# Performance work log

Hardware: AMD Instinct MI355X
Metric: run time of the kernel (lower is better)

The kernel has to match this reference:

```python
import jax, jax.numpy as jnp
import numpy as np

HIDDEN = 4096
N_HEADS = 32
N_KV_HEADS = 8
HEAD_DIM = HIDDEN // N_HEADS  # 128
GROUPS = N_HEADS // N_KV_HEADS  # 4
ROPE_BASE = 10000.0
BATCH, SEQ = 1, 2048


def _rope_cos_sin(position_ids, dim, base):
    # position_ids: [b, s] int -> cos/sin [b, s, dim]
    inv_freq = 1.0 / (base ** (jnp.arange(0, dim, 2, dtype=jnp.float32) / dim))  # [dim/2]
    freqs = position_ids.astype(jnp.float32)[..., None] * inv_freq  # [b, s, dim/2]
    emb = jnp.concatenate([freqs, freqs], axis=-1)  # [b, s, dim]
    return jnp.cos(emb), jnp.sin(emb)


def _rotate_half(x):
    x1, x2 = jnp.split(x, 2, axis=-1)
    return jnp.concatenate([-x2, x1], axis=-1)


def setup_inputs() -> dict:
    key = jax.random.key(0)
    ks = jax.random.split(key, 8)
    s = 0.02
    return {
        'hidden_states': jax.random.normal(ks[0], (BATCH, SEQ, HIDDEN), dtype=jnp.float32),
        'position_ids': jnp.broadcast_to(jnp.arange(SEQ, dtype=jnp.int64), (BATCH, SEQ)),
        'Wq': jax.random.normal(ks[1], (HIDDEN, N_HEADS * HEAD_DIM), dtype=jnp.float32) * s,
        'bq': jax.random.normal(ks[2], (N_HEADS * HEAD_DIM,), dtype=jnp.float32) * s,
        'Wk': jax.random.normal(ks[3], (HIDDEN, N_KV_HEADS * HEAD_DIM), dtype=jnp.float32) * s,
        'bk': jax.random.normal(ks[4], (N_KV_HEADS * HEAD_DIM,), dtype=jnp.float32) * s,
        'Wv': jax.random.normal(ks[5], (HIDDEN, N_KV_HEADS * HEAD_DIM), dtype=jnp.float32) * s,
        'bv': jax.random.normal(ks[6], (N_KV_HEADS * HEAD_DIM,), dtype=jnp.float32) * s,
        'Wo': jax.random.normal(ks[7], (HIDDEN, HIDDEN), dtype=jnp.float32) * s,
    }


def reference(hidden_states, position_ids, Wq, bq, Wk, bk, Wv, bv, Wo):
    b, s, _ = hidden_states.shape
    # QKV projections (bias=True for q/k/v per module)
    q = hidden_states @ Wq + bq  # [b, s, H*d]
    k = hidden_states @ Wk + bk  # [b, s, Hk*d]
    v = hidden_states @ Wv + bv  # [b, s, Hk*d]
    q = q.reshape(b, s, N_HEADS, HEAD_DIM)
    k = k.reshape(b, s, N_KV_HEADS, HEAD_DIM)
    v = v.reshape(b, s, N_KV_HEADS, HEAD_DIM)

    # RoPE gathered by position_ids
    cos, sin = _rope_cos_sin(position_ids, HEAD_DIM, ROPE_BASE)  # [b, s, d]
    cos = cos[:, :, None, :]
    sin = sin[:, :, None, :]
    q = q * cos + _rotate_half(q) * sin
    k = k * cos + _rotate_half(k) * sin

    # GQA causal attention: group query heads over shared kv heads
    qg = q.reshape(b, s, N_KV_HEADS, GROUPS, HEAD_DIM)
    scale = 1.0 / jnp.sqrt(jnp.asarray(HEAD_DIM, dtype=q.dtype))
    scores = jnp.einsum('bqhgd,bkhd->bhgqk', qg, k) * scale  # [b, Hk, g, s, s]
    causal = jnp.tril(jnp.ones((s, s), dtype=bool))
    scores = jnp.where(causal, scores, jnp.finfo(scores.dtype).min)
    probs = jax.nn.softmax(scores, axis=-1)
    out = jnp.einsum('bhgqk,bkhd->bqhgd', probs, v)  # [b, s, Hk, g, d]
    out = out.reshape(b, s, HIDDEN)
    return out @ Wo  # o_proj, bias=False
```

## Files before the change

### kernel.cpp

```cpp
#include <hip/hip_runtime.h>
#include <hip/hip_bf16.h>

typedef __hip_bfloat16 bf16;
typedef __attribute__((ext_vector_type(8))) __bf16 bf16x8;
typedef __attribute__((ext_vector_type(4))) float f32x4;

#define SEQ 2048
#define HID 4096
#define NH 32
#define NKV 8
#define HD 128
#define KVDIM 1024
#define QKVN 6144

#define MiB (1024 * 1024)
#define SCALE_LOG2E 0.12751743f

__device__ __forceinline__ void gl_lds16(const void* g, void* lds) {
  __builtin_amdgcn_global_load_lds((const __attribute__((address_space(1))) void*)g,
                                   (__attribute__((address_space(3))) void*)lds,
                                   16, 0, 0);
}

__device__ __forceinline__ float unplo(unsigned u) { return __uint_as_float(u << 16); }
__device__ __forceinline__ float unphi(unsigned u) { return __uint_as_float(u & 0xffff0000u); }
__device__ __forceinline__ unsigned packbf(float a, float b) {
  bf16 t[2] = {__float2bfloat16(a), __float2bfloat16(b)};
  return *reinterpret_cast<unsigned*>(t);
}

__global__ void concat_bias_kernel(const float* __restrict__ bq, const float* __restrict__ bk,
                                   const float* __restrict__ bv, float* __restrict__ o) {
  int i = blockIdx.x * blockDim.x + threadIdx.x;
  if (i >= QKVN) return;
  o[i] = (i < HID) ? bq[i] : (i < HID + KVDIM ? bk[i - HID] : bv[i - HID - KVDIM]);
}

__global__ void transpose_all_kernel(const float* __restrict__ Wq, const float* __restrict__ Wk,
                                     const float* __restrict__ Wv, const float* __restrict__ Wo,
                                     bf16* __restrict__ Wqkvt, bf16* __restrict__ Wot,
                                     const float* __restrict__ hidden, bf16* __restrict__ Xb) {
  __shared__ float tile[32][33];
  int t = blockIdx.x;
  if (t >= 40960) {
    int i = ((t - 40960) * 256 + threadIdx.y * 32 + threadIdx.x) * 4;
    float4 v = *reinterpret_cast<const float4*>(hidden + i);
    bf16 o[4] = {__float2bfloat16(v.x), __float2bfloat16(v.y),
                 __float2bfloat16(v.z), __float2bfloat16(v.w)};
    *reinterpret_cast<short4*>(Xb + i) = *reinterpret_cast<const short4*>(o);
    return;
  }
  const float* in;
  bf16* out;
  int si, xt, yt;
  if (t < 16384)      { in = Wq; out = Wqkvt;                           si = HID;   xt = t & 127; yt = t >> 7; }
  else if (t < 20480) { t -= 16384; in = Wk; out = Wqkvt + (size_t)HID * HID;           si = KVDIM; xt = t & 31; yt = t >> 5; }
  else if (t < 24576) { t -= 20480; in = Wv; out = Wqkvt + (size_t)(HID + KVDIM) * HID; si = KVDIM; xt = t & 31; yt = t >> 5; }
  else                { t -= 24576; in = Wo; out = Wot;                 si = HID;   xt = t & 127; yt = t >> 7; }
  int c0 = xt * 32, r0 = yt * 32;
  int tx = threadIdx.x, ty = threadIdx.y;
#pragma unroll
  for (int i = 0; i < 32; i += 8)
    tile[ty + i][tx] = in[(size_t)(r0 + ty + i) * si + (c0 + tx)];
  __syncthreads();
#pragma unroll
  for (int i = 0; i < 32; i += 8)
    out[(size_t)(c0 + ty + i) * HID + (r0 + tx)] = __float2bfloat16(tile[tx][ty + i]);
}

__global__ void postqkv_kernel(const bf16* __restrict__ Ch, bf16* __restrict__ Qb,
                               bf16* __restrict__ Kb, bf16* __restrict__ Vt) {
  __shared__ float tile[32][33];
  int b = blockIdx.x;
  int tid = threadIdx.x;
  if (b < 10240) {
    bool isQ = (b < 8192);
    int idx = (isQ ? b : b - 8192) * 256 + tid;
    int j = idx & 31;
    int h = (idx >> 5) & (isQ ? 31 : 7);
    int s = idx >> (isQ ? 10 : 8);
    size_t bi = (size_t)s * QKVN + (isQ ? 0 : HID) + h * HD;
    unsigned u1 = *reinterpret_cast<const unsigned*>(Ch + bi + 2 * j);
    unsigned u2 = *reinterpret_cast<const unsigned*>(Ch + bi + 64 + 2 * j);
    float x1a = unplo(u1), x1b = unphi(u1);
    float x2a = unplo(u2), x2b = unphi(u2);
    float inv0 = __expf(-(float)(2 * j) * 0.14391156831212787f);
    float inv1 = __expf(-(float)(2 * j + 1) * 0.14391156831212787f);
    float sn0, cs0, sn1, cs1;
    __sincosf((float)s * inv0, &sn0, &cs0);
    __sincosf((float)s * inv1, &sn1, &cs1);
    if (isQ) {
      cs0 *= SCALE_LOG2E; sn0 *= SCALE_LOG2E;
      cs1 *= SCALE_LOG2E; sn1 *= SCALE_LOG2E;
    }
    size_t bo = (size_t)s * (isQ ? HID : KVDIM) + h * HD;
    bf16* Ob = isQ ? Qb : Kb;
    *reinterpret_cast<unsigned*>(Ob + bo + 2 * j) =
        packbf(x1a * cs0 - x2a * sn0, x1b * cs1 - x2b * sn1);
    *reinterpret_cast<unsigned*>(Ob + bo + 64 + 2 * j) =
        packbf(x2a * cs0 + x1a * sn0, x2b * cs1 + x1b * sn1);
  } else {
    int t = b - 10240;
    int xt = t & 31, yt = t >> 5;
    int tx = tid & 31, ty = tid >> 5;
#pragma unroll
    for (int i = 0; i < 32; i += 8)
      tile[ty + i][tx] = __bfloat162float(Ch[(size_t)(yt * 32 + ty + i) * QKVN + (HID + KVDIM) + xt * 32 + tx]);
    __syncthreads();
#pragma unroll
    for (int i = 0; i < 32; i += 8)
      Vt[(size_t)(xt * 32 + ty + i) * SEQ + (yt * 32 + tx)] = __float2bfloat16(tile[tx][ty + i]);
  }
}

#define BARRIER() __builtin_amdgcn_s_barrier()
#define LGKM0()                                          \
  {                                                      \
    asm volatile("s_waitcnt lgkmcnt(0)" ::: "memory");   \
    __builtin_amdgcn_sched_barrier(0);                   \
  }
#define MFMA_ACC(d, x, y) d = __builtin_amdgcn_mfma_f32_16x16x32_bf16(x, y, d, 0, 0, 0)

__global__ __launch_bounds__(512, 2) void qkvgemm_kernel(
    const bf16* __restrict__ A,
    const bf16* __restrict__ Bt,
    const float* __restrict__ bias,
    bf16* __restrict__ Ch) {
  __shared__ bf16 lds[2][448 * 64];
  const int blk = blockIdx.x;
  const int sw = (blk & 7) * 32 + (blk >> 3);
  const int bx = sw & 31, by = sw >> 5;
  const int n0 = bx * 192;
  const int m0 = by * 256;
  const int tid = threadIdx.x;
  const int lane = tid & 63;
  const int w = tid >> 6;
  const int wr = w >> 2, wc = w & 3;
  const int hig = lane >> 4;
  const int nt = HID / 64;

#define QSTAGE_A(buf, t)                                                          \
  {                                                                               \
    _Pragma("unroll")                                                             \
    for (int _c = 0; _c < 4; ++_c) {                                              \
      int _row = _c * 64 + w * 8 + (lane >> 3);                                   \
      int _ch = (lane & 7) ^ ((lane >> 3) & 7);                                   \
      gl_lds16(A + (size_t)(m0 + _row) * HID + (size_t)(t) * 64 + _ch * 8,        \
               &lds[buf][(_c * 64 + w * 8) * 64]);                                \
    }                                                                             \
  }
#define QSTAGE_B(buf, t)                                                          \
  {                                                                               \
    _Pragma("unroll")                                                             \
    for (int _c = 0; _c < 3; ++_c) {                                              \
      int _row = _c * 64 + w * 8 + (lane >> 3);                                   \
      int _ch = (lane & 7) ^ ((lane >> 3) & 7);                                   \
      gl_lds16(Bt + (size_t)(n0 + _row) * HID + (size_t)(t) * 64 + _ch * 8,       \
               &lds[buf][(256 + _c * 64 + w * 8) * 64]);                          \
    }                                                                             \
  }

  auto rdA = [&](int cur, int mi, int ks) {
    int rr = wr * 128 + mi * 16 + (lane & 15);
    int byt = rr * 128 + (((ks * 32 + hig * 8) * 2) ^ ((rr & 7) << 4));
    return *reinterpret_cast<const bf16x8*>(
        reinterpret_cast<const char*>(&lds[cur][0]) + byt);
  };
  auto rdB = [&](int cur, int ni, int ks) {
    int rr = wc * 48 + ni * 16 + (lane & 15);
    int byt = 32768 + rr * 128 + (((ks * 32 + hig * 8) * 2) ^ ((rr & 7) << 4));
    return *reinterpret_cast<const bf16x8*>(
        reinterpret_cast<const char*>(&lds[cur][0]) + byt);
  };

  f32x4 acc[8][3];
  const f32x4 z = {0.f, 0.f, 0.f, 0.f};
#pragma unroll
  for (int i = 0; i < 8; ++i)
#pragma unroll
    for (int j = 0; j < 3; ++j) acc[i][j] = z;

  QSTAGE_A(0, 0); QSTAGE_B(0, 0);
  QSTAGE_B(1, 1);
  asm volatile("s_waitcnt vmcnt(3)" ::: "memory");
  BARRIER();

  bf16x8 a[4][2], b[3][2];
  int cur = 0;
  for (int t = 0; t < nt; ++t, cur ^= 1) {
#pragma unroll
    for (int mi = 0; mi < 4; ++mi) { a[mi][0] = rdA(cur, mi, 0); a[mi][1] = rdA(cur, mi, 1); }
#pragma unroll
    for (int ni = 0; ni < 3; ++ni) { b[ni][0] = rdB(cur, ni, 0); b[ni][1] = rdB(cur, ni, 1); }
    if (t + 1 < nt) QSTAGE_A(cur ^ 1, t + 1);
    LGKM0();
    __builtin_amdgcn_s_setprio(1);
#pragma unroll
    for (int mi = 0; mi < 4; ++mi)
#pragma unroll
      for (int ni = 0; ni < 3; ++ni) {
        MFMA_ACC(acc[mi][ni], a[mi][0], b[ni][0]);
        MFMA_ACC(acc[mi][ni], a[mi][1], b[ni][1]);
      }
    __builtin_amdgcn_s_setprio(0);
    BARRIER();
#pragma unroll
    for (int mi = 0; mi < 4; ++mi) { a[mi][0] = rdA(cur, mi + 4, 0); a[mi][1] = rdA(cur, mi + 4, 1); }
    if (t + 2 < nt) QSTAGE_B(cur, t + 2);
    LGKM0();
    __builtin_amdgcn_s_setprio(1);
#pragma unroll
    for (int mi = 0; mi < 4; ++mi)
#pragma unroll
      for (int ni = 0; ni < 3; ++ni) {
        MFMA_ACC(acc[mi + 4][ni], a[mi][0], b[ni][0]);
        MFMA_ACC(acc[mi + 4][ni], a[mi][1], b[ni][1]);
      }
    __builtin_amdgcn_s_setprio(0);
    if (t + 1 < nt) {
      if (t + 2 < nt) {
        asm volatile("s_waitcnt vmcnt(3)" ::: "memory");
      } else {
        asm volatile("s_waitcnt vmcnt(0)" ::: "memory");
      }
    }
    BARRIER();
  }

#pragma unroll
  for (int ni = 0; ni < 3; ++ni) {
    int col = n0 + wc * 48 + ni * 16 + (lane & 15);
    float bv = bias[col];
#pragma unroll
    for (int mi = 0; mi < 8; ++mi) {
      int rbase = m0 + wr * 128 + mi * 16 + hig * 4;
#pragma unroll
      for (int r = 0; r < 4; ++r)
        Ch[(size_t)(rbase + r) * QKVN + col] = __float2bfloat16(acc[mi][ni][r] + bv);
    }
  }
#undef QSTAGE_A
#undef QSTAGE_B
}

__global__ __launch_bounds__(512, 2) void wogemm_kernel(
    const bf16* __restrict__ A,
    const bf16* __restrict__ Bt,
    float* __restrict__ C) {
  __shared__ bf16 lds[2][3][128 * 64];
  const int blk = blockIdx.x;
  const int sw = (blk & 7) * 32 + (blk >> 3);
  const int n0 = (sw & 31) * 128;
  const int m0 = (sw >> 5) * 256;
  const int tid = threadIdx.x;
  const int lane = tid & 63;
  const int w = tid >> 6;
  const int wr = w >> 1, wc = w & 1;
  const int nt = HID / 64;

#define WSTAGE(buf, slot, t)                                                    \
  {                                                                             \
    const bf16* _s = ((slot) == 2) ? Bt : A;                                    \
    int _g0 = ((slot) == 2) ? n0 : (m0 + (slot) * 128);                         \
    _Pragma("unroll")                                                           \
    for (int _it = 0; _it < 2; ++_it) {                                         \
      int _row = w * 16 + _it * 8 + (lane >> 3);                                \
      int _ch = (lane & 7) ^ (_row & 7);                                        \
      gl_lds16(_s + (size_t)(_g0 + _row) * HID + (size_t)(t) * 64 + _ch * 8,    \
               &lds[buf][slot][(w * 16 + _it * 8) * 64]);                       \
    }                                                                           \
  }

  auto rdA = [&](int cur, int mi, int ks) {
    int rr = (wr & 1) * 64 + mi * 16 + (lane & 15);
    int byt = rr * 128 + (((ks * 32 + (lane >> 4) * 8) * 2) ^ ((rr & 7) << 4));
    return *reinterpret_cast<const bf16x8*>(
        reinterpret_cast<const char*>(&lds[cur][wr >> 1][0]) + byt);
  };
  auto rdB = [&](int cur, int ni, int ks) {
    int rr = wc * 64 + ni * 16 + (lane & 15);
    int byt = rr * 128 + (((ks * 32 + (lane >> 4) * 8) * 2) ^ ((rr & 7) << 4));
    return *reinterpret_cast<const bf16x8*>(
        reinterpret_cast<const char*>(&lds[cur][2][0]) + byt);
  };

  f32x4 acc[4][4];
  const f32x4 z = {0.f, 0.f, 0.f, 0.f};
#pragma unroll
  for (int i = 0; i < 4; ++i)
#pragma unroll
    for (int j = 0; j < 4; ++j) acc[i][j] = z;

  WSTAGE(0, 0, 0); WSTAGE(0, 1, 0); WSTAGE(0, 2, 0);
  WSTAGE(1, 2, 1);
  asm volatile("s_waitcnt vmcnt(2)" ::: "memory");
  BARRIER();

  bf16x8 a[2][2], b[4][2];
  int cur = 0;
  for (int t = 0; t < nt; ++t, cur ^= 1) {
#pragma unroll
    for (int mi = 0; mi < 2; ++mi) { a[mi][0] = rdA(cur, mi, 0); a[mi][1] = rdA(cur, mi, 1); }
#pragma unroll
    for (int ni = 0; ni < 4; ++ni) { b[ni][0] = rdB(cur, ni, 0); b[ni][1] = rdB(cur, ni, 1); }
    if (t + 1 < nt) { WSTAGE(cur ^ 1, 0, t + 1); WSTAGE(cur ^ 1, 1, t + 1); }
    LGKM0();
    __builtin_amdgcn_s_setprio(1);
#pragma unroll
    for (int mi = 0; mi < 2; ++mi)
#pragma unroll
      for (int ni = 0; ni < 4; ++ni) {
        MFMA_ACC(acc[mi][ni], a[mi][0], b[ni][0]);
        MFMA_ACC(acc[mi][ni], a[mi][1], b[ni][1]);
      }
    __builtin_amdgcn_s_setprio(0);
    BARRIER();
#pragma unroll
    for (int mi = 0; mi < 2; ++mi) { a[mi][0] = rdA(cur, mi + 2, 0); a[mi][1] = rdA(cur, mi + 2, 1); }
    if (t + 2 < nt) WSTAGE(cur, 2, t + 2);
    LGKM0();
    __builtin_amdgcn_s_setprio(1);
#pragma unroll
    for (int mi = 0; mi < 2; ++mi)
#pragma unroll
      for (int ni = 0; ni < 4; ++ni) {
        MFMA_ACC(acc[mi + 2][ni], a[mi][0], b[ni][0]);
        MFMA_ACC(acc[mi + 2][ni], a[mi][1], b[ni][1]);
      }
    __builtin_amdgcn_s_setprio(0);
    if (t + 1 < nt) {
      if (t + 2 < nt) {
        asm volatile("s_waitcnt vmcnt(2)" ::: "memory");
      } else {
        asm volatile("s_waitcnt vmcnt(0)" ::: "memory");
      }
    }
    BARRIER();
  }

#pragma unroll
  for (int ni = 0; ni < 4; ++ni) {
    int col = n0 + wc * 64 + ni * 16 + (lane & 15);
#pragma unroll
    for (int mi = 0; mi < 4; ++mi) {
      int rbase = m0 + wr * 64 + mi * 16 + (lane >> 4) * 4;
#pragma unroll
      for (int r = 0; r < 4; ++r)
        C[(size_t)(rbase + r) * HID + col] = acc[mi][ni][r];
    }
  }
#undef WSTAGE
}

__global__ __launch_bounds__(256) void attn_kernel(
    const bf16* __restrict__ Q, const bf16* __restrict__ Kb,
    const bf16* __restrict__ Vt, bf16* __restrict__ AO,
    float* __restrict__ Opart, float* __restrict__ Ml) {
  __shared__ bf16 Ks[64 * 128];
  __shared__ bf16 Vs[128 * 64];
  __shared__ bf16 Ps[4][16 * 64];
  const int tid = threadIdx.x, lane = tid & 63, w = tid >> 6;
  const int b = blockIdx.x;
  const int H = b & 31;
  const int tt = b >> 5;
  int qb, lo, hi, half;
  bool split;
  if (tt < 32) {
    qb = 16 + ((31 - tt) >> 1);
    half = tt & 1;
    int n = qb + 1, mid = n >> 1;
    lo = half ? mid : 0;
    hi = half ? n : mid;
    split = true;
  } else {
    qb = 47 - tt;
    half = 0;
    lo = 0;
    hi = qb + 1;
    split = false;
  }
  const int kvh = H >> 2;
  const int qw = qb * 64 + w * 16;
  const int hig = lane >> 4;
  const int q_loc = lane & 15;
  const int qa = qw + q_loc;

  bf16x8 aq[4];
#pragma unroll
  for (int kd = 0; kd < 4; ++kd) {
    int row = qw + q_loc;
    int d = kd * 32 + hig * 8;
    aq[kd] = *reinterpret_cast<const bf16x8*>(Q + (size_t)row * HID + H * HD + d);
  }

  float m_run = -1e30f, l_run = 0.0f;
  f32x4 o[8];
  const f32x4 z = {0.f, 0.f, 0.f, 0.f};
#pragma unroll
  for (int dt = 0; dt < 8; ++dt) o[dt] = z;

  for (int t = lo; t < hi; ++t) {
    int kvbase = t * 64;
#pragma unroll
    for (int it = 0; it < 4; ++it) {
      int c = w * 4 + it;
      int row = c * 4 + (lane >> 4);
      int sb = ((lane & 15) * 16) ^ ((row & 7) << 4);
      gl_lds16(Kb + (size_t)(kvbase + row) * KVDIM + kvh * HD + (sb >> 1), &Ks[c * 512]);
    }
#pragma unroll
    for (int it = 0; it < 4; ++it) {
      int c = w * 4 + it;
      int row = c * 8 + (lane >> 3);
      int sb = ((lane & 7) * 16) ^ ((row & 7) << 4);
      gl_lds16(Vt + (size_t)(kvh * HD + row) * SEQ + kvbase + (sb >> 1), &Vs[c * 512]);
    }
    __syncthreads();

    f32x4 sf[4];
#pragma unroll
    for (int j = 0; j < 4; ++j) sf[j] = z;
#pragma unroll
    for (int j = 0; j < 4; ++j) {
#pragma unroll
      for (int kd = 0; kd < 4; ++kd) {
        int r = j * 16 + q_loc;
        int byt = r * 256 + (((kd * 32 + hig * 8) * 2) ^ ((r & 7) << 4));
        bf16x8 kfr = *reinterpret_cast<const bf16x8*>(reinterpret_cast<const char*>(Ks) + byt);
        sf[j] = __builtin_amdgcn_mfma_f32_16x16x32_bf16(kfr, aq[kd], sf[j], 0, 0, 0);
      }
    }

    float vals[4][4];
    bool diag = (t == qb);
#pragma unroll
    for (int j = 0; j < 4; ++j)
#pragma unroll
      for (int r = 0; r < 4; ++r) {
        float v = sf[j][r];
        if (diag) {
          int ka = kvbase + j * 16 + hig * 4 + r;
          if (ka > qa) v = -1e30f;
        }
        vals[j][r] = v;
      }

    float m01 = fmaxf(fmaxf(vals[0][0], vals[0][1]), fmaxf(vals[0][2], vals[0][3]));
    float m23 = fmaxf(fmaxf(vals[1][0], vals[1][1]), fmaxf(vals[1][2], vals[1][3]));
    float m45 = fmaxf(fmaxf(vals[2][0], vals[2][1]), fmaxf(vals[2][2], vals[2][3]));
    float m67 = fmaxf(fmaxf(vals[3][0], vals[3][1]), fmaxf(vals[3][2], vals[3][3]));
    float m = fmaxf(fmaxf(m01, m23), fmaxf(m45, m67));
    m = fmaxf(m, __shfl_xor(m, 16));
    m = fmaxf(m, __shfl_xor(m, 32));
    float m_old = m_run;
    float mn = fmaxf(m_old, m);
    m_run = mn;
    float alpha = __builtin_exp2f(m_old - mn);

    float p[4][4];
    float rs = 0.0f;
#pragma unroll
    for (int j = 0; j < 4; ++j)
#pragma unroll
      for (int r = 0; r < 4; ++r) {
        p[j][r] = __builtin_exp2f(vals[j][r] - mn);
        rs += p[j][r];
      }
    rs += __shfl_xor(rs, 16);
    rs += __shfl_xor(rs, 32);
    l_run = l_run * alpha + rs;

#pragma unroll
    for (int j = 0; j < 4; ++j) {
      bf16 tmp[4] = {__float2bfloat16(p[j][0]), __float2bfloat16(p[j][1]),
                     __float2bfloat16(p[j][2]), __float2bfloat16(p[j][3])};
      int coff = (j * 16 + hig * 4) * 2;
      int byt = q_loc * 128 + (coff ^ ((q_loc & 7) << 4));
      *reinterpret_cast<uint2*>(reinterpret_cast<char*>(&Ps[w][0]) + byt) =
          *reinterpret_cast<const uint2*>(tmp);
    }

    if (__any(mn > m_old)) {
#pragma unroll
      for (int r = 0; r < 4; ++r) {
        float alr = __shfl(alpha, hig * 4 + r);
#pragma unroll
        for (int dt = 0; dt < 8; ++dt) o[dt][r] *= alr;
      }
    }

    bf16x8 pa[2];
#pragma unroll
    for (int ks = 0; ks < 2; ++ks) {
      int byt = q_loc * 128 + (((ks * 32 + hig * 8) * 2) ^ ((q_loc & 7) << 4));
      pa[ks] = *reinterpret_cast<const bf16x8*>(reinterpret_cast<const char*>(&Ps[w][0]) + byt);
    }
#pragma unroll
    for (int dt = 0; dt < 8; ++dt)
#pragma unroll
      for (int ks = 0; ks < 2; ++ks) {
        int vrow = dt * 16 + q_loc;
        int byt = vrow * 128 + (((ks * 32 + hig * 8) * 2) ^ ((vrow & 7) << 4));
        bf16x8 vb = *reinterpret_cast<const bf16x8*>(reinterpret_cast<const char*>(Vs) + byt);
        o[dt] = __builtin_amdgcn_mfma_f32_16x16x32_bf16(pa[ks], vb, o[dt], 0, 0, 0);
      }
    __syncthreads();
  }

  if (!split) {
#pragma unroll
    for (int r = 0; r < 4; ++r) {
      float li = __shfl(l_run, hig * 4 + r);
      float linv = 1.0f / li;
#pragma unroll
      for (int dt = 0; dt < 8; ++dt) {
        int qrow = qw + hig * 4 + r;
        int d = dt * 16 + q_loc;
        AO[(size_t)qrow * HID + H * HD + d] = __float2bfloat16(o[dt][r] * linv);
      }
    }
  } else {
    size_t pbase = ((size_t)(half * NH + H) * 1024);
#pragma unroll
    for (int dt = 0; dt < 8; ++dt)
#pragma unroll
      for (int r = 0; r < 4; ++r) {
        int qrow = qw + hig * 4 + r;
        int d = dt * 16 + q_loc;
        Opart[(pbase + (qrow - 1024)) * HD + d] = o[dt][r];
      }
    if (lane < 16) {
      Ml[(pbase + (qa - 1024)) * 2 + 0] = m_run;
      Ml[(pbase + (qa - 1024)) * 2 + 1] = l_run;
    }
  }
}

__global__ __launch_bounds__(256) void merge_kernel(
    const float* __restrict__ Opart, const float* __restrict__ Ml,
    bf16* __restrict__ AO) {
  int i = blockIdx.x * 256 + threadIdx.x;
  int dq = (i & 31) << 2;
  int row = (i >> 5) & 1023;
  int H = i >> 15;
  size_t b1 = (size_t)H * 1024 + row;
  size_t b2 = (size_t)(NH + H) * 1024 + row;
  float m1 = Ml[b1 * 2], l1 = Ml[b1 * 2 + 1];
  float m2 = Ml[b2 * 2], l2 = Ml[b2 * 2 + 1];
  float M = fmaxf(m1, m2);
  float w1 = __builtin_exp2f(m1 - M), w2 = __builtin_exp2f(m2 - M);
  float inv = 1.0f / (l1 * w1 + l2 * w2);
  float4 o1 = *reinterpret_cast<const float4*>(Opart + b1 * HD + dq);
  float4 o2 = *reinterpret_cast<const float4*>(Opart + b2 * HD + dq);
  bf16 o[4] = {__float2bfloat16((o1.x * w1 + o2.x * w2) * inv),
               __float2bfloat16((o1.y * w1 + o2.y * w2) * inv),
               __float2bfloat16((o1.z * w1 + o2.z * w2) * inv),
               __float2bfloat16((o1.w * w1 + o2.w * w2) * inv)};
  *reinterpret_cast<short4*>(AO + (size_t)(1024 + row) * HID + H * HD + dq) =
      *reinterpret_cast<const short4*>(o);
}

extern "C" void kernel_launch(void* const* d_in, const int* in_sizes, int n_in,
                              void* d_out, int out_size, void* d_ws, size_t ws_size,
                              hipStream_t stream) {
  const float* hidden = (const float*)d_in[0];
  const float* Wq = (const float*)d_in[2];
  const float* bq = (const float*)d_in[3];
  const float* Wk = (const float*)d_in[4];
  const float* bk = (const float*)d_in[5];
  const float* Wv = (const float*)d_in[6];
  const float* bv = (const float*)d_in[7];
  const float* Wo = (const float*)d_in[8];
  float* out = (float*)d_out;

  char* ws = (char*)d_ws;
  bf16*  Wqkvt  = (bf16*)(ws + (size_t)0 * MiB);
  bf16*  Xb     = (bf16*)(ws + (size_t)48 * MiB);
  bf16*  Cqkvh  = (bf16*)(ws + (size_t)64 * MiB);
  bf16*  Wot    = (bf16*)(ws + (size_t)88 * MiB);
  bf16*  Qb     = (bf16*)(ws + (size_t)120 * MiB);
  bf16*  Kb     = (bf16*)(ws + (size_t)136 * MiB);
  bf16*  Vt     = (bf16*)(ws + (size_t)140 * MiB);
  float* bqkv   = (float*)Qb;
  bf16*  AO     = Cqkvh;
  float* Opart  = (float*)Wqkvt;
  float* Ml     = (float*)(ws + (size_t)48 * MiB);

  concat_bias_kernel<<<QKVN / 256, 256, 0, stream>>>(bq, bk, bv, bqkv);
  transpose_all_kernel<<<49152, dim3(32, 8), 0, stream>>>(
      Wq, Wk, Wv, Wo, Wqkvt, Wot, hidden, Xb);

  qkvgemm_kernel<<<256, 512, 0, stream>>>(Xb, Wqkvt, bqkv, Cqkvh);

  postqkv_kernel<<<12288, 256, 0, stream>>>(Cqkvh, Qb, Kb, Vt);

  attn_kernel<<<1536, 256, 0, stream>>>(Qb, Kb, Vt, AO, Opart, Ml);
  merge_kernel<<<(NH * 1024 * 32) / 256, 256, 0, stream>>>(Opart, Ml, AO);

  wogemm_kernel<<<256, 512, 0, stream>>>(AO, Wot, out);
}
```

Before: 317.3 us.

## Replace split-KV attention with paired query-block scheduling and drop merge kernel

The attention work split changes. Before, long query blocks were split into two KV halves with partial outputs merged by a separate kernel. Now each block processes a pair of query blocks (pr and 31-pr) in two sequential passes, which gives every block the same causal work. This removes the fp32 partial writes, the merge kernel launch and its memory traffic. In exchange the grid shrinks from 1536 to 512 blocks, each running longer serial loops, which may reduce occupancy and latency hiding on 256 CUs.

```diff
diff --git a/kernel.cpp b/kernel.cpp
--- a/kernel.cpp
+++ b/kernel.cpp
@@ -354,160 +354,146 @@
 
 __global__ __launch_bounds__(256) void attn_kernel(
     const bf16* __restrict__ Q, const bf16* __restrict__ Kb,
-    const bf16* __restrict__ Vt, bf16* __restrict__ AO,
-    float* __restrict__ Opart, float* __restrict__ Ml) {
+    const bf16* __restrict__ Vt, bf16* __restrict__ AO) {
   __shared__ bf16 Ks[64 * 128];
   __shared__ bf16 Vs[128 * 64];
   __shared__ bf16 Ps[4][16 * 64];
   const int tid = threadIdx.x, lane = tid & 63, w = tid >> 6;
   const int b = blockIdx.x;
   const int H = b & 31;
-  const int tt = b >> 5;
-  int qb, lo, hi, half;
-  bool split;
-  if (tt < 32) {
-    qb = 16 + ((31 - tt) >> 1);
-    half = tt & 1;
-    int n = qb + 1, mid = n >> 1;
-    lo = half ? mid : 0;
-    hi = half ? n : mid;
-    split = true;
-  } else {
-    qb = 47 - tt;
-    half = 0;
-    lo = 0;
-    hi = qb + 1;
-    split = false;
-  }
+  const int pr = b >> 5;
   const int kvh = H >> 2;
-  const int qw = qb * 64 + w * 16;
   const int hig = lane >> 4;
   const int q_loc = lane & 15;
-  const int qa = qw + q_loc;
-
-  bf16x8 aq[4];
-#pragma unroll
-  for (int kd = 0; kd < 4; ++kd) {
-    int row = qw + q_loc;
-    int d = kd * 32 + hig * 8;
-    aq[kd] = *reinterpret_cast<const bf16x8*>(Q + (size_t)row * HID + H * HD + d);
-  }
-
-  float m_run = -1e30f, l_run = 0.0f;
-  f32x4 o[8];
   const f32x4 z = {0.f, 0.f, 0.f, 0.f};
-#pragma unroll
-  for (int dt = 0; dt < 8; ++dt) o[dt] = z;
-
-  for (int t = lo; t < hi; ++t) {
-    int kvbase = t * 64;
-#pragma unroll
-    for (int it = 0; it < 4; ++it) {
-      int c = w * 4 + it;
-      int row = c * 4 + (lane >> 4);
-      int sb = ((lane & 15) * 16) ^ ((row & 7) << 4);
-      gl_lds16(Kb + (size_t)(kvbase + row) * KVDIM + kvh * HD + (sb >> 1), &Ks[c * 512]);
-    }
-#pragma unroll
-    for (int it = 0; it < 4; ++it) {
-      int c = w * 4 + it;
-      int row = c * 8 + (lane >> 3);
-      int sb = ((lane & 7) * 16) ^ ((row & 7) << 4);
-      gl_lds16(Vt + (size_t)(kvh * HD + row) * SEQ + kvbase + (sb >> 1), &Vs[c * 512]);
-    }
-    __syncthreads();
-
-    f32x4 sf[4];
-#pragma unroll
-    for (int j = 0; j < 4; ++j) sf[j] = z;
-#pragma unroll
-    for (int j = 0; j < 4; ++j) {
-#pragma unroll
-      for (int kd = 0; kd < 4; ++kd) {
-        int r = j * 16 + q_loc;
-        int byt = r * 256 + (((kd * 32 + hig * 8) * 2) ^ ((r & 7) << 4));
-        bf16x8 kfr = *reinterpret_cast<const bf16x8*>(reinterpret_cast<const char*>(Ks) + byt);
-        sf[j] = __builtin_amdgcn_mfma_f32_16x16x32_bf16(kfr, aq[kd], sf[j], 0, 0, 0);
-      }
-    }
-
-    float vals[4][4];
-    bool diag = (t == qb);
-#pragma unroll
-    for (int j = 0; j < 4; ++j)
-#pragma unroll
-      for (int r = 0; r < 4; ++r) {
-        float v = sf[j][r];
-        if (diag) {
-          int ka = kvbase + j * 16 + hig * 4 + r;
-          if (ka > qa) v = -1e30f;
+
+#pragma unroll
+  for (int pass = 0; pass < 2; ++pass) {
+    const int qb = pass ? (31 - pr) : pr;
+    const int qw = qb * 64 + w * 16;
+    const int qa = qw + q_loc;
+
+    bf16x8 aq[4];
+#pragma unroll
+    for (int kd = 0; kd < 4; ++kd) {
+      int row = qw + q_loc;
+      int d = kd * 32 + hig * 8;
+      aq[kd] = *reinterpret_cast<const bf16x8*>(Q + (size_t)row * HID + H * HD + d);
+    }
+
+    float m_run = -1e30f, l_run = 0.0f;
+    f32x4 o[8];
+#pragma unroll
+    for (int dt = 0; dt < 8; ++dt) o[dt] = z;
+
+    for (int t = 0; t <= qb; ++t) {
+      int kvbase = t * 64;
+#pragma unroll
+      for (int it = 0; it < 4; ++it) {
+        int c = w * 4 + it;
+        int row = c * 4 + (lane >> 4);
+        int sb = ((lane & 15) * 16) ^ ((row & 7) << 4);
+        gl_lds16(Kb + (size_t)(kvbase + row) * KVDIM + kvh * HD + (sb >> 1), &Ks[c * 512]);
+      }
+#pragma unroll
+      for (int it = 0; it < 4; ++it) {
+        int c = w * 4 + it;
+        int row = c * 8 + (lane >> 3);
+        int sb = ((lane & 7) * 16) ^ ((row & 7) << 4);
+        gl_lds16(Vt + (size_t)(kvh * HD + row) * SEQ + kvbase + (sb >> 1), &Vs[c * 512]);
+      }
+      __syncthreads();
+
+      f32x4 sf[4];
+#pragma unroll
+      for (int j = 0; j < 4; ++j) sf[j] = z;
+#pragma unroll
+      for (int j = 0; j < 4; ++j) {
+#pragma unroll
+        for (int kd = 0; kd < 4; ++kd) {
+          int r = j * 16 + q_loc;
+          int byt = r * 256 + (((kd * 32 + hig * 8) * 2) ^ ((r & 7) << 4));
+          bf16x8 kfr = *reinterpret_cast<const bf16x8*>(reinterpret_cast<const char*>(Ks) + byt);
+          sf[j] = __builtin_amdgcn_mfma_f32_16x16x32_bf16(kfr, aq[kd], sf[j], 0, 0, 0);
         }
-        vals[j][r] = v;
-      }
-
-    float m01 = fmaxf(fmaxf(vals[0][0], vals[0][1]), fmaxf(vals[0][2], vals[0][3]));
-    float m23 = fmaxf(fmaxf(vals[1][0], vals[1][1]), fmaxf(vals[1][2], vals[1][3]));
-    float m45 = fmaxf(fmaxf(vals[2][0], vals[2][1]), fmaxf(vals[2][2], vals[2][3]));
-    float m67 = fmaxf(fmaxf(vals[3][0], vals[3][1]), fmaxf(vals[3][2], vals[3][3]));
-    float m = fmaxf(fmaxf(m01, m23), fmaxf(m45, m67));
-    m = fmaxf(m, __shfl_xor(m, 16));
-    m = fmaxf(m, __shfl_xor(m, 32));
-    float m_old = m_run;
-    float mn = fmaxf(m_old, m);
-    m_run = mn;
-    float alpha = __builtin_exp2f(m_old - mn);
-
-    float p[4][4];
-    float rs = 0.0f;
-#pragma unroll
-    for (int j = 0; j < 4; ++j)
-#pragma unroll
-      for (int r = 0; r < 4; ++r) {
-        p[j][r] = __builtin_exp2f(vals[j][r] - mn);
-        rs += p[j][r];
-      }
-    rs += __shfl_xor(rs, 16);
-    rs += __shfl_xor(rs, 32);
-    l_run = l_run * alpha + rs;
-
-#pragma unroll
-    for (int j = 0; j < 4; ++j) {
-      bf16 tmp[4] = {__float2bfloat16(p[j][0]), __float2bfloat16(p[j][1]),
-                     __float2bfloat16(p[j][2]), __float2bfloat16(p[j][3])};
-      int coff = (j * 16 + hig * 4) * 2;
-      int byt = q_loc * 128 + (coff ^ ((q_loc & 7) << 4));
-      *reinterpret_cast<uint2*>(reinterpret_cast<char*>(&Ps[w][0]) + byt) =
-          *reinterpret_cast<const uint2*>(tmp);
-    }
-
-    if (__any(mn > m_old)) {
-#pragma unroll
-      for (int r = 0; r < 4; ++r) {
-        float alr = __shfl(alpha, hig * 4 + r);
-#pragma unroll
-        for (int dt = 0; dt < 8; ++dt) o[dt][r] *= alr;
-      }
-    }
-
-    bf16x8 pa[2];
-#pragma unroll
-    for (int ks = 0; ks < 2; ++ks) {
-      int byt = q_loc * 128 + (((ks * 32 + hig * 8) * 2) ^ ((q_loc & 7) << 4));
-      pa[ks] = *reinterpret_cast<const bf16x8*>(reinterpret_cast<const char*>(&Ps[w][0]) + byt);
-    }
-#pragma unroll
-    for (int dt = 0; dt < 8; ++dt)
+      }
+
+      float vals[4][4];
+      bool diag = (t == qb);
+#pragma unroll
+      for (int j = 0; j < 4; ++j)
+#pragma unroll
+        for (int r = 0; r < 4; ++r) {
+          float v = sf[j][r];
+          if (diag) {
+            int ka = kvbase + j * 16 + hig * 4 + r;
+            if (ka > qa) v = -1e30f;
+          }
+          vals[j][r] = v;
+        }
+
+      float m01 = fmaxf(fmaxf(vals[0][0], vals[0][1]), fmaxf(vals[0][2], vals[0][3]));
+      float m23 = fmaxf(fmaxf(vals[1][0], vals[1][1]), fmaxf(vals[1][2], vals[1][3]));
+      float m45 = fmaxf(fmaxf(vals[2][0], vals[2][1]), fmaxf(vals[2][2], vals[2][3]));
+      float m67 = fmaxf(fmaxf(vals[3][0], vals[3][1]), fmaxf(vals[3][2], vals[3][3]));
+      float m = fmaxf(fmaxf(m01, m23), fmaxf(m45, m67));
+      m = fmaxf(m, __shfl_xor(m, 16));
+      m = fmaxf(m, __shfl_xor(m, 32));
+      float m_old = m_run;
+      float mn = fmaxf(m_old, m);
+      m_run = mn;
+      float alpha = __builtin_exp2f(m_old - mn);
+
+      float p[4][4];
+      float rs = 0.0f;
+#pragma unroll
+      for (int j = 0; j < 4; ++j)
+#pragma unroll
+        for (int r = 0; r < 4; ++r) {
+          p[j][r] = __builtin_exp2f(vals[j][r] - mn);
+          rs += p[j][r];
+        }
+      rs += __shfl_xor(rs, 16);
+      rs += __shfl_xor(rs, 32);
+      l_run = l_run * alpha + rs;
+
+#pragma unroll
+      for (int j = 0; j < 4; ++j) {
+        bf16 tmp[4] = {__float2bfloat16(p[j][0]), __float2bfloat16(p[j][1]),
+                       __float2bfloat16(p[j][2]), __float2bfloat16(p[j][3])};
+        int coff = (j * 16 + hig * 4) * 2;
+        int byt = q_loc * 128 + (coff ^ ((q_loc & 7) << 4));
+        *reinterpret_cast<uint2*>(reinterpret_cast<char*>(&Ps[w][0]) + byt) =
+            *reinterpret_cast<const uint2*>(tmp);
+      }
+
+      if (__any(mn > m_old)) {
+#pragma unroll
+        for (int r = 0; r < 4; ++r) {
+          float alr = __shfl(alpha, hig * 4 + r);
+#pragma unroll
+          for (int dt = 0; dt < 8; ++dt) o[dt][r] *= alr;
+        }
+      }
+
+      bf16x8 pa[2];
 #pragma unroll
       for (int ks = 0; ks < 2; ++ks) {
-        int vrow = dt * 16 + q_loc;
-        int byt = vrow * 128 + (((ks * 32 + hig * 8) * 2) ^ ((vrow & 7) << 4));
-        bf16x8 vb = *reinterpret_cast<const bf16x8*>(reinterpret_cast<const char*>(Vs) + byt);
-        o[dt] = __builtin_amdgcn_mfma_f32_16x16x32_bf16(pa[ks], vb, o[dt], 0, 0, 0);
-      }
-    __syncthreads();
-  }
-
-  if (!split) {
+        int byt = q_loc * 128 + (((ks * 32 + hig * 8) * 2) ^ ((q_loc & 7) << 4));
+        pa[ks] = *reinterpret_cast<const bf16x8*>(reinterpret_cast<const char*>(&Ps[w][0]) + byt);
+      }
+#pragma unroll
+      for (int dt = 0; dt < 8; ++dt)
+#pragma unroll
+        for (int ks = 0; ks < 2; ++ks) {
+          int vrow = dt * 16 + q_loc;
+          int byt = vrow * 128 + (((ks * 32 + hig * 8) * 2) ^ ((vrow & 7) << 4));
+          bf16x8 vb = *reinterpret_cast<const bf16x8*>(reinterpret_cast<const char*>(Vs) + byt);
+          o[dt] = __builtin_amdgcn_mfma_f32_16x16x32_bf16(pa[ks], vb, o[dt], 0, 0, 0);
+        }
+      __syncthreads();
+    }
+
 #pragma unroll
     for (int r = 0; r < 4; ++r) {
       float li = __shfl(l_run, hig * 4 + r);
@@ -519,45 +505,7 @@
         AO[(size_t)qrow * HID + H * HD + d] = __float2bfloat16(o[dt][r] * linv);
       }
     }
-  } else {
-    size_t pbase = ((size_t)(half * NH + H) * 1024);
-#pragma unroll
-    for (int dt = 0; dt < 8; ++dt)
-#pragma unroll
-      for (int r = 0; r < 4; ++r) {
-        int qrow = qw + hig * 4 + r;
-        int d = dt * 16 + q_loc;
-        Opart[(pbase + (qrow - 1024)) * HD + d] = o[dt][r];
-      }
-    if (lane < 16) {
-      Ml[(pbase + (qa - 1024)) * 2 + 0] = m_run;
-      Ml[(pbase + (qa - 1024)) * 2 + 1] = l_run;
-    }
-  }
-}
-
-__global__ __launch_bounds__(256) void merge_kernel(
-    const float* __restrict__ Opart, const float* __restrict__ Ml,
-    bf16* __restrict__ AO) {
-  int i = blockIdx.x * 256 + threadIdx.x;
-  int dq = (i & 31) << 2;
-  int row = (i >> 5) & 1023;
-  int H = i >> 15;
-  size_t b1 = (size_t)H * 1024 + row;
-  size_t b2 = (size_t)(NH + H) * 1024 + row;
-  float m1 = Ml[b1 * 2], l1 = Ml[b1 * 2 + 1];
-  float m2 = Ml[b2 * 2], l2 = Ml[b2 * 2 + 1];
-  float M = fmaxf(m1, m2);
-  float w1 = __builtin_exp2f(m1 - M), w2 = __builtin_exp2f(m2 - M);
-  float inv = 1.0f / (l1 * w1 + l2 * w2);
-  float4 o1 = *reinterpret_cast<const float4*>(Opart + b1 * HD + dq);
-  float4 o2 = *reinterpret_cast<const float4*>(Opart + b2 * HD + dq);
-  bf16 o[4] = {__float2bfloat16((o1.x * w1 + o2.x * w2) * inv),
-               __float2bfloat16((o1.y * w1 + o2.y * w2) * inv),
-               __float2bfloat16((o1.z * w1 + o2.z * w2) * inv),
-               __float2bfloat16((o1.w * w1 + o2.w * w2) * inv)};
-  *reinterpret_cast<short4*>(AO + (size_t)(1024 + row) * HID + H * HD + dq) =
-      *reinterpret_cast<const short4*>(o);
+  }
 }
 
 extern "C" void kernel_launch(void* const* d_in, const int* in_sizes, int n_in,
@@ -583,8 +531,6 @@
   bf16*  Vt     = (bf16*)(ws + (size_t)140 * MiB);
   float* bqkv   = (float*)Qb;
   bf16*  AO     = Cqkvh;
-  float* Opart  = (float*)Wqkvt;
-  float* Ml     = (float*)(ws + (size_t)48 * MiB);
 
   concat_bias_kernel<<<QKVN / 256, 256, 0, stream>>>(bq, bk, bv, bqkv);
   transpose_all_kernel<<<49152, dim3(32, 8), 0, stream>>>(
@@ -594,8 +540,7 @@
 
   postqkv_kernel<<<12288, 256, 0, stream>>>(Cqkvh, Qb, Kb, Vt);
 
-  attn_kernel<<<1536, 256, 0, stream>>>(Qb, Kb, Vt, AO, Opart, Ml);
-  merge_kernel<<<(NH * 1024 * 32) / 256, 256, 0, stream>>>(Opart, Ml, AO);
+  attn_kernel<<<512, 256, 0, stream>>>(Qb, Kb, Vt, AO);
 
   wogemm_kernel<<<256, 512, 0, stream>>>(AO, Wot, out);
 }
```

After: 310.0 us. 1.02x faster.
